# Optimization experiments

Measured on AMD Instinct MI355X. Metric: run time of the kernel, lower is better.

## Reference

```python
import jax, jax.numpy as jnp
import numpy as np

B, T, D = 8, 8192, 256
H = 16            # history_length
K = 3             # neighbor kernel_size
DECAY = 0.9
EPS = 1e-5


def _layernorm(x, g, b):
    m = jnp.mean(x, axis=-1, keepdims=True)
    v = jnp.var(x, axis=-1, keepdims=True)
    return (x - m) * jax.lax.rsqrt(v + EPS) * g + b


def _window_weighted_sum(x_pad, weights, seq_len):
    # sum_j w[j] * x_pad[:, j:j+T, :] -- fixed-weight local aggregation,
    # avoids materializing the [B,T,W,D] unfold tensor.
    out = weights[0] * x_pad[:, 0:seq_len, :]
    for j in range(1, weights.shape[0]):
        out = out + weights[j] * x_pad[:, j:j + seq_len, :]
    return out


def temporal_weights():
    w = DECAY ** np.arange(H, dtype=np.float32)
    return jnp.asarray(w / w.sum())


def setup_inputs() -> dict:
    key = jax.random.key(0)
    ks = jax.random.split(key, 16)
    s = 1.0 / np.sqrt(D)
    s2 = 1.0 / np.sqrt(2 * D)
    inp = {
        "x": jax.random.normal(ks[0], (B, T, D), jnp.float32),
        # LayerNorms
        "n1_g": jnp.ones((D,), jnp.float32), "n1_b": jnp.zeros((D,), jnp.float32),
        "n2_g": jnp.ones((D,), jnp.float32), "n2_b": jnp.zeros((D,), jnp.float32),
        "n3_g": jnp.ones((D,), jnp.float32), "n3_b": jnp.zeros((D,), jnp.float32),
        # temporal value/out proj (stored as [in,out])
        "t_Wv": jax.random.uniform(ks[1], (D, D), jnp.float32, -s, s),
        "t_bv": jax.random.uniform(ks[2], (D,), jnp.float32, -s, s),
        "t_Wo": jax.random.uniform(ks[3], (D, D), jnp.float32, -s, s),
        "t_bo": jax.random.uniform(ks[4], (D,), jnp.float32, -s, s),
        # neighbor value/out proj
        "a_Wv": jax.random.uniform(ks[5], (D, D), jnp.float32, -s, s),
        "a_bv": jax.random.uniform(ks[6], (D,), jnp.float32, -s, s),
        "a_Wo": jax.random.uniform(ks[7], (D, D), jnp.float32, -s, s),
        "a_bo": jax.random.uniform(ks[8], (D,), jnp.float32, -s, s),
        # FFN
        "f_W1": jax.random.uniform(ks[9], (D, 2 * D), jnp.float32, -s, s),
        "f_b1": jax.random.uniform(ks[10], (2 * D,), jnp.float32, -s, s),
        "f_W2": jax.random.uniform(ks[11], (2 * D, D), jnp.float32, -s2, s2),
        "f_b2": jax.random.uniform(ks[12], (D,), jnp.float32, -s2, s2),
    }
    return inp


def reference(x, n1_g, n1_b, n2_g, n2_b, n3_g, n3_b,
              t_Wv, t_bv, t_Wo, t_bo,
              a_Wv, a_bv, a_Wo, a_bo,
              f_W1, f_b1, f_W2, f_b2):
    # --- temporal memory: causal fixed exponential-decay window ---
    h = _layernorm(x, n1_g, n1_b)
    h_pad = jnp.pad(h, ((0, 0), (H - 1, 0), (0, 0)))  # zeros on the left
    tw = temporal_weights()  # tw[j] weights the j-th-oldest element (decay^j)
    agg = _window_weighted_sum(h_pad, tw, T)
    # weights sum to 1 => weighted-sum-of-linear == linear-of-weighted-sum
    attended = agg @ t_Wv + t_bv
    x = x + (attended @ t_Wo + t_bo)

    # --- neighbor attention: [t-1, t, t+1] uniform window, replicate pad ---
    h = _layernorm(x, n2_g, n2_b)
    h_pad = jnp.pad(h, ((0, 0), (1, 1), (0, 0)), mode="edge")
    nw = jnp.full((K,), 1.0 / K, jnp.float32)
    agg = _window_weighted_sum(h_pad, nw, T)
    attended = agg @ a_Wv + a_bv
    x = x + (attended @ a_Wo + a_bo)

    # --- FFN (dropout is identity at eval) ---
    h = _layernorm(x, n3_g, n3_b)
    h = jax.nn.gelu(h @ f_W1 + f_b1, approximate=False)
    x = x + (h @ f_W2 + f_b2)
    return x
```

## Files before the change

kernel.cpp:

```cpp
#include <hip/hip_runtime.h>
#include <cstdint>
#include <cstddef>

#define TT 8192
#define BB 8
#define DD 256
#define NTOK (BB * TT)

typedef unsigned short u16;
typedef unsigned int u32;

typedef __attribute__((ext_vector_type(8))) short bf16x8;
typedef __attribute__((ext_vector_type(4))) float f32x4;

__device__ __forceinline__ float bf2f(u16 u) {
    u32 v = ((u32)u) << 16;
    float f;
    __builtin_memcpy(&f, &v, 4);
    return f;
}

__device__ __forceinline__ u16 f2bf(float f) {
    u32 v;
    __builtin_memcpy(&v, &f, 4);
    u32 r = (v + 0x7FFFu + ((v >> 16) & 1u)) >> 16;
    return (u16)r;
}

__device__ __forceinline__ uint2 pack4(const float* v) {
    uint2 p;
    p.x = (u32)f2bf(v[0]) | ((u32)f2bf(v[1]) << 16);
    p.y = (u32)f2bf(v[2]) | ((u32)f2bf(v[3]) << 16);
    return p;
}

__device__ __forceinline__ void unpack4(uint2 p, float* v) {
    v[0] = bf2f((u16)(p.x & 0xFFFFu));
    v[1] = bf2f((u16)(p.x >> 16));
    v[2] = bf2f((u16)(p.y & 0xFFFFu));
    v[3] = bf2f((u16)(p.y >> 16));
}

__device__ __forceinline__ uint4 pack8(const float* v) {
    uint4 p;
    p.x = (u32)f2bf(v[0]) | ((u32)f2bf(v[1]) << 16);
    p.y = (u32)f2bf(v[2]) | ((u32)f2bf(v[3]) << 16);
    p.z = (u32)f2bf(v[4]) | ((u32)f2bf(v[5]) << 16);
    p.w = (u32)f2bf(v[6]) | ((u32)f2bf(v[7]) << 16);
    return p;
}

__device__ __forceinline__ void unpack8(uint4 p, float* v) {
    v[0] = bf2f((u16)(p.x & 0xFFFFu));
    v[1] = bf2f((u16)(p.x >> 16));
    v[2] = bf2f((u16)(p.y & 0xFFFFu));
    v[3] = bf2f((u16)(p.y >> 16));
    v[4] = bf2f((u16)(p.z & 0xFFFFu));
    v[5] = bf2f((u16)(p.z >> 16));
    v[6] = bf2f((u16)(p.w & 0xFFFFu));
    v[7] = bf2f((u16)(p.w >> 16));
}

__global__ __launch_bounds__(256) void k_diag(float* out, float code) {
    out[(size_t)blockIdx.x * 256 + threadIdx.x] = code;
}

__global__ __launch_bounds__(256) void k_transpose(
    const float* s0, const float* s1, const float* s2, const float* s3,
    const float* s4, const float* s5,
    u16* d0, u16* d1, u16* d2, u16* d3, u16* d4, u16* d5) {
    const int z = blockIdx.z;
    const float* src;
    u16* dst;
    int K, N, tr;
    switch (z) {
        case 0: src = s0; dst = d0; K = 256; N = 256; tr = 1; break;
        case 1: src = s1; dst = d1; K = 256; N = 256; tr = 1; break;
        case 2: src = s2; dst = d2; K = 256; N = 512; tr = 1; break;
        case 3: src = s3; dst = d3; K = 512; N = 256; tr = 1; break;
        case 4: src = s4; dst = d4; K = 256; N = 256; tr = 0; break;
        default: src = s5; dst = d5; K = 256; N = 256; tr = 0; break;
    }
    const int nb = blockIdx.x * 32, kb = blockIdx.y * 32;
    if (nb >= N || kb >= K) return;
    const int tx = threadIdx.x & 31, ty = threadIdx.x >> 5;
    if (!tr) {
        for (int i = ty; i < 32; i += 8)
            dst[(size_t)(kb + i) * N + nb + tx] =
                f2bf(src[(size_t)(kb + i) * N + nb + tx]);
        return;
    }
    __shared__ u16 tile[32][33];
    for (int i = ty; i < 32; i += 8)
        tile[i][tx] = f2bf(src[(size_t)(kb + i) * N + nb + tx]);
    __syncthreads();
    for (int i = ty; i < 32; i += 8)
        dst[(size_t)(nb + i) * K + kb + tx] = tile[tx][i];
}

__global__ __launch_bounds__(256) void k_bias_compose(
    const float* tbv, const float* tWo, const float* tbo,
    const float* abv, const float* aWo, const float* abo,
    float* bc1, float* bc2) {
    const float* bv = blockIdx.x ? abv : tbv;
    const float* Wo = blockIdx.x ? aWo : tWo;
    const float* bo = blockIdx.x ? abo : tbo;
    float* bc = blockIdx.x ? bc2 : bc1;
    const int n = threadIdx.x;
    float s = bo[n];
    for (int j = 0; j < 256; j++) s += bv[j] * Wo[j * 256 + n];
    bc[n] = s;
}

__global__ __launch_bounds__(256) void k_ln_temporal(
    const float* __restrict__ x, const float* __restrict__ gw,
    const float* __restrict__ bw, u16* __restrict__ out) {
    const int b = blockIdx.y;
    const int t0 = blockIdx.x * 64;
    const int tid = threadIdx.x;
    const int wv = tid >> 6, lane = tid & 63;
    const int d4 = lane * 4;
    __shared__ u16 hl[79 * 256];

    const float4 gv = *(const float4*)(gw + d4);
    const float4 bv = *(const float4*)(bw + d4);

    for (int i = wv; i < 79; i += 4) {
        const int t = t0 + i - 15;
        if (t < 0) {
            *(uint2*)(hl + i * 256 + d4) = make_uint2(0u, 0u);
            continue;
        }
        const float4 v = *(const float4*)(x + ((size_t)b * TT + t) * DD + d4);
        float s = v.x + v.y + v.z + v.w;
        float ss = v.x * v.x + v.y * v.y + v.z * v.z + v.w * v.w;
        for (int m = 1; m < 64; m <<= 1) {
            s += __shfl_xor(s, m);
            ss += __shfl_xor(ss, m);
        }
        const float mean = s * (1.0f / 256.0f);
        const float var = ss * (1.0f / 256.0f) - mean * mean;
        const float rs = rsqrtf(fmaxf(var, 0.f) + 1e-5f);
        float h[4] = {(v.x - mean) * rs * gv.x + bv.x,
                      (v.y - mean) * rs * gv.y + bv.y,
                      (v.z - mean) * rs * gv.z + bv.z,
                      (v.w - mean) * rs * gv.w + bv.w};
        *(uint2*)(hl + i * 256 + d4) = pack4(h);
    }
    __syncthreads();

    float tw[16];
    {
        float p = 1.f, s = 0.f;
        for (int j = 0; j < 16; j++) {
            tw[j] = p;
            s += p;
            p *= 0.9f;
        }
        const float inv = 1.f / s;
        for (int j = 0; j < 16; j++) tw[j] *= inv;
    }
    const int dc = (tid & 63) * 4;
    const int tg = (tid >> 6) * 16;
    for (int ot = tg; ot < tg + 16; ++ot) {
        float a[4] = {0.f, 0.f, 0.f, 0.f};
        for (int j = 0; j < 16; j++) {
            float h[4];
            unpack4(*(const uint2*)(hl + (ot + j) * 256 + dc), h);
            a[0] += tw[j] * h[0];
            a[1] += tw[j] * h[1];
            a[2] += tw[j] * h[2];
            a[3] += tw[j] * h[3];
        }
        *(uint2*)(out + ((size_t)b * TT + t0 + ot) * DD + dc) = pack4(a);
    }
}

__global__ __launch_bounds__(256) void k_gemm_prep(
    const u16* __restrict__ A, const u16* __restrict__ Wt,
    u16* out, int M, int K, int Nc, int ldw) {
    const int m0 = blockIdx.y * 128;
    const int n0 = blockIdx.x * 128;
    const int tid = threadIdx.x;
    const int wv = tid >> 6, lane = tid & 63;
    const int quad = lane >> 4, l16 = lane & 15;
    const int wm = (wv >> 1) * 64, wn = (wv & 1) * 64;

    __shared__ u16 lA[128 * 40];
    __shared__ u16 lB[128 * 40];

    f32x4 acc[4][4];
#pragma unroll
    for (int i = 0; i < 4; i++)
#pragma unroll
        for (int j = 0; j < 4; j++) acc[i][j] = (f32x4){0.f, 0.f, 0.f, 0.f};

    const int r = tid >> 2;
    const int c = tid & 3;

    for (int k0 = 0; k0 < K; k0 += 32) {
        __syncthreads();
        {
            const uint4 a0 = *(const uint4*)(A + (size_t)(m0 + r) * K + k0 + c * 8);
            const uint4 a1 = *(const uint4*)(A + (size_t)(m0 + r + 64) * K + k0 + c * 8);
            const uint4 b0 = *(const uint4*)(Wt + (size_t)(n0 + r) * ldw + k0 + c * 8);
            const uint4 b1 = *(const uint4*)(Wt + (size_t)(n0 + r + 64) * ldw + k0 + c * 8);
            *(uint4*)(lA + r * 40 + c * 8) = a0;
            *(uint4*)(lA + (r + 64) * 40 + c * 8) = a1;
            *(uint4*)(lB + r * 40 + c * 8) = b0;
            *(uint4*)(lB + (r + 64) * 40 + c * 8) = b1;
        }
        __syncthreads();
        bf16x8 af[4], bfr[4];
#pragma unroll
        for (int i = 0; i < 4; i++)
            af[i] = *(const bf16x8*)(lA + (wm + i * 16 + l16) * 40 + quad * 8);
#pragma unroll
        for (int j = 0; j < 4; j++)
            bfr[j] = *(const bf16x8*)(lB + (wn + j * 16 + l16) * 40 + quad * 8);
#pragma unroll
        for (int i = 0; i < 4; i++)
#pragma unroll
            for (int j = 0; j < 4; j++)
                acc[i][j] = __builtin_amdgcn_mfma_f32_16x16x32_bf16(
                    af[i], bfr[j], acc[i][j], 0, 0, 0);
    }

#pragma unroll
    for (int i = 0; i < 4; i++) {
        const int rowb = m0 + wm + i * 16 + quad * 4;
#pragma unroll
        for (int j = 0; j < 4; j++) {
            const int col = n0 + wn + j * 16 + l16;
#pragma unroll
            for (int rr = 0; rr < 4; rr++)
                out[(size_t)(rowb + rr) * Nc + col] = f2bf(acc[i][j][rr]);
        }
    }
}

template <int AMODE, int RES, int GELU, int SF32, int LNOUT>
__global__ __launch_bounds__(256) void k_mega(
    const u16* __restrict__ A, const u16* __restrict__ A2, int K,
    const u16* __restrict__ Wt, int ldw, const float* __restrict__ bias,
    const float* res, float* outf, u16* __restrict__ outh,
    const float* __restrict__ lng, const float* __restrict__ lnb,
    u16* __restrict__ hout) {
    const int m0 = blockIdx.x * 64;
    const int t = threadIdx.x;
    const int lane = t & 63, wv = t >> 6;
    const int quad = lane >> 4, l16 = lane & 15;
    const int wn = wv * 64;

    __shared__ u16 sA[66 * 40];
    __shared__ u16 sA2[AMODE ? 64 * 40 : 8];
    __shared__ float sBuf[5120];
    u16* sB = (u16*)sBuf;
    float* sE = sBuf;
    __shared__ float sMean[16], sRstd[16];
    __shared__ float sG[LNOUT ? 256 : 1], sBl[LNOUT ? 256 : 1];

    if (LNOUT) {
        sG[t] = lng[t];
        sBl[t] = lnb[t];
    }

    f32x4 acc[4][4];
#pragma unroll
    for (int i = 0; i < 4; i++)
#pragma unroll
        for (int j = 0; j < 4; j++) acc[i][j] = (f32x4){0.f, 0.f, 0.f, 0.f};

    int rowLo = 0, rowHi = 0;
    if (AMODE) {
        rowLo = (m0 % TT == 0) ? m0 : m0 - 1;
        rowHi = ((m0 + 64) % TT == 0) ? (m0 + 63) : (m0 + 64);
    }

    const int ar = t >> 2, ac8 = (t & 3) * 8;
    for (int k0 = 0; k0 < K; k0 += 32) {
        const u16* Asrc = (k0 >= 256) ? A2 : A;
        const int kk = k0 & 255;
        __syncthreads();
        if (AMODE == 0) {
            *(uint4*)(sA + ar * 40 + ac8) =
                *(const uint4*)(Asrc + (size_t)(m0 + ar) * 256 + kk + ac8);
        } else {
            *(uint4*)(sA + (ar + 1) * 40 + ac8) =
                *(const uint4*)(Asrc + (size_t)(m0 + ar) * 256 + kk + ac8);
            if (t < 8) {
                const int hr = (t >> 2) ? rowHi : rowLo;
                const int dr = (t >> 2) ? 65 : 0;
                *(uint4*)(sA + dr * 40 + (t & 3) * 8) =
                    *(const uint4*)(Asrc + (size_t)hr * 256 + kk + (t & 3) * 8);
            }
        }
#pragma unroll
        for (int q = 0; q < 4; q++) {
            const int ch = t + q * 256;
            *(uint4*)(sB + (ch >> 2) * 40 + (ch & 3) * 8) =
                *(const uint4*)(Wt + (size_t)(ch >> 2) * ldw + k0 + (ch & 3) * 8);
        }
        __syncthreads();
        if (AMODE) {
            float v0[8], v1[8], v2[8], o[8];
            unpack8(*(const uint4*)(sA + ar * 40 + ac8), v0);
            unpack8(*(const uint4*)(sA + (ar + 1) * 40 + ac8), v1);
            unpack8(*(const uint4*)(sA + (ar + 2) * 40 + ac8), v2);
#pragma unroll
            for (int e = 0; e < 8; e++)
                o[e] = (v0[e] + v1[e] + v2[e]) * (1.0f / 3.0f);
            *(uint4*)(sA2 + ar * 40 + ac8) = pack8(o);
            __syncthreads();
        }
        const u16* Af = AMODE ? sA2 : sA;
        bf16x8 af[4], bfr[4];
#pragma unroll
        for (int i = 0; i < 4; i++)
            af[i] = *(const bf16x8*)(Af + (i * 16 + l16) * 40 + quad * 8);
#pragma unroll
        for (int j = 0; j < 4; j++)
            bfr[j] = *(const bf16x8*)(sB + (wn + j * 16 + l16) * 40 + quad * 8);
#pragma unroll
        for (int i = 0; i < 4; i++)
#pragma unroll
            for (int j = 0; j < 4; j++)
                acc[i][j] = __builtin_amdgcn_mfma_f32_16x16x32_bf16(
                    af[i], bfr[j], acc[i][j], 0, 0, 0);
    }

    float bvl[4];
#pragma unroll
    for (int j = 0; j < 4; j++) bvl[j] = bias[wn + j * 16 + l16];

    const int row = t >> 4;
    const int colb = (t & 15) * 16;
    for (int cch = 0; cch < 4; cch++) {
        const int gr = m0 + cch * 16 + row;
        __syncthreads();
        if (RES) {
            const float* rp = res + (size_t)gr * 256 + colb;
            float* sp = sE + row * 268 + colb;
#pragma unroll
            for (int q = 0; q < 4; q++)
                *(float4*)(sp + q * 4) = *(const float4*)(rp + q * 4);
        }
        __syncthreads();
        {
#pragma unroll
            for (int j = 0; j < 4; j++) {
#pragma unroll
                for (int rr = 0; rr < 4; rr++) {
                    const int rl = quad * 4 + rr;
                    const int ad = rl * 268 + wn + j * 16 + l16;
                    float v = acc[cch][j][rr] + bvl[j];
                    if (RES) v += sE[ad];
                    if (GELU)
                        v = 0.5f * v * (1.0f + erff(v * 0.70710678118654752f));
                    sE[ad] = v;
                }
            }
        }
        __syncthreads();
        if (LNOUT) {
#pragma unroll
            for (int r4 = 0; r4 < 4; r4++) {
                const int rl = wv * 4 + r4;
                const float4 vv = *(const float4*)(sE + rl * 268 + lane * 4);
                float s = vv.x + vv.y + vv.z + vv.w;
                float ss = vv.x * vv.x + vv.y * vv.y + vv.z * vv.z + vv.w * vv.w;
                for (int m = 1; m < 64; m <<= 1) {
                    s += __shfl_xor(s, m);
                    ss += __shfl_xor(ss, m);
                }
                if (lane == 0) {
                    const float mean = s * (1.0f / 256.0f);
                    const float var = ss * (1.0f / 256.0f) - mean * mean;
                    sMean[rl] = mean;
                    sRstd[rl] = rsqrtf(fmaxf(var, 0.f) + 1e-5f);
                }
            }
            __syncthreads();
        }
        const float* sp = sE + row * 268 + colb;
        if (SF32) {
            float* op = outf + (size_t)gr * 256 + colb;
#pragma unroll
            for (int q = 0; q < 4; q++)
                *(float4*)(op + q * 4) = *(const float4*)(sp + q * 4);
        }
        if (GELU) {
            u16* op = outh + (size_t)gr * 256 + colb;
            *(uint4*)op = pack8(sp);
            *(uint4*)(op + 8) = pack8(sp + 8);
        }
        if (LNOUT) {
            const float m = sMean[row], rs = sRstd[row];
            float h[16];
#pragma unroll
            for (int e = 0; e < 16; e++)
                h[e] = (sp[e] - m) * rs * sG[colb + e] + sBl[colb + e];
            u16* hp = hout + (size_t)gr * 256 + colb;
            *(uint4*)hp = pack8(h);
            *(uint4*)(hp + 8) = pack8(h + 8);
        }
    }
}

__global__ __launch_bounds__(256) void k_ffn(
    const u16* __restrict__ A,
    const u16* __restrict__ W1T,
    const float* __restrict__ b1,
    const u16* __restrict__ W2T,
    const float* __restrict__ b2,
    const float* res,
    float* out) {
    const int m0 = blockIdx.x * 64;
    const int t = threadIdx.x;
    const int lane = t & 63, wv = t >> 6;
    const int quad = lane >> 4, l16 = lane & 15;

    __shared__ u16 sA[8 * 64 * 40];
    __shared__ u16 sT[64 * 72];
    float* sE = (float*)sA;

#pragma unroll
    for (int q = 0; q < 8; q++) {
        const int id = q * 256 + t;
        const int arow = id >> 5;
        const int c8 = (id & 31) * 8;
        const int ks = c8 >> 5;
        const int kc = c8 & 31;
        *(uint4*)(sA + (ks * 64 + arow) * 40 + kc) =
            *(const uint4*)(A + (size_t)(m0 + arow) * 256 + c8);
    }

    f32x4 acc2[4][4];
#pragma unroll
    for (int i = 0; i < 4; i++)
#pragma unroll
        for (int jj = 0; jj < 4; jj++) acc2[i][jj] = (f32x4){0.f, 0.f, 0.f, 0.f};

    __syncthreads();

    for (int j = 0; j < 8; j++) {
        const int n1 = j * 64 + wv * 16 + l16;
        bf16x8 bw[8];
#pragma unroll
        for (int ks = 0; ks < 8; ks++)
            bw[ks] = *(const bf16x8*)(W1T + (size_t)n1 * 256 + ks * 32 + quad * 8);
        f32x4 acc1[4];
#pragma unroll
        for (int i = 0; i < 4; i++) acc1[i] = (f32x4){0.f, 0.f, 0.f, 0.f};
#pragma unroll
        for (int ks = 0; ks < 8; ks++) {
#pragma unroll
            for (int i = 0; i < 4; i++) {
                const bf16x8 af = *(const bf16x8*)(
                    sA + (ks * 64 + i * 16 + l16) * 40 + quad * 8);
                acc1[i] = __builtin_amdgcn_mfma_f32_16x16x32_bf16(
                    af, bw[ks], acc1[i], 0, 0, 0);
            }
        }
        const float b1l = b1[n1];
#pragma unroll
        for (int i = 0; i < 4; i++)
#pragma unroll
            for (int rr = 0; rr < 4; rr++) {
                float v = acc1[i][rr] + b1l;
                v = 0.5f * v * (1.0f + erff(v * 0.70710678118654752f));
                sT[(i * 16 + quad * 4 + rr) * 72 + wv * 16 + l16] = f2bf(v);
            }
        __syncthreads();
#pragma unroll
        for (int kh = 0; kh < 2; kh++) {
            bf16x8 bw2[4];
#pragma unroll
            for (int jj = 0; jj < 4; jj++)
                bw2[jj] = *(const bf16x8*)(
                    W2T + (size_t)(wv * 64 + jj * 16 + l16) * 512 + j * 64 +
                    kh * 32 + quad * 8);
#pragma unroll
            for (int i = 0; i < 4; i++) {
                const bf16x8 af = *(const bf16x8*)(
                    sT + (i * 16 + l16) * 72 + kh * 32 + quad * 8);
#pragma unroll
                for (int jj = 0; jj < 4; jj++)
                    acc2[i][jj] = __builtin_amdgcn_mfma_f32_16x16x32_bf16(
                        af, bw2[jj], acc2[i][jj], 0, 0, 0);
            }
        }
        __syncthreads();
    }

    float bvl[4];
#pragma unroll
    for (int jj = 0; jj < 4; jj++) bvl[jj] = b2[wv * 64 + jj * 16 + l16];
    const int row = t >> 4;
    const int colb = (t & 15) * 16;
    for (int cch = 0; cch < 4; cch++) {
        const int gr = m0 + cch * 16 + row;
        __syncthreads();
        {
            const float* rp = res + (size_t)gr * 256 + colb;
            float* sp = sE + row * 268 + colb;
#pragma unroll
            for (int q = 0; q < 4; q++)
                *(float4*)(sp + q * 4) = *(const float4*)(rp + q * 4);
        }
        __syncthreads();
#pragma unroll
        for (int jj = 0; jj < 4; jj++)
#pragma unroll
            for (int rr = 0; rr < 4; rr++) {
                const int ad = (quad * 4 + rr) * 268 + wv * 64 + jj * 16 + l16;
                sE[ad] += acc2[cch][jj][rr] + bvl[jj];
            }
        __syncthreads();
        {
            float* op = out + (size_t)gr * 256 + colb;
            const float* sp = sE + row * 268 + colb;
#pragma unroll
            for (int q = 0; q < 4; q++)
                *(float4*)(op + q * 4) = *(const float4*)(sp + q * 4);
        }
    }
}

extern "C" void kernel_launch(void* const* d_in, const int* in_sizes, int n_in,
                              void* d_out, int out_size, void* d_ws,
                              size_t ws_size, hipStream_t stream) {
    const float* x = (const float*)d_in[0];
    const float* n1g = (const float*)d_in[1];
    const float* n1b = (const float*)d_in[2];
    const float* n2g = (const float*)d_in[3];
    const float* n2b = (const float*)d_in[4];
    const float* n3g = (const float*)d_in[5];
    const float* n3b = (const float*)d_in[6];
    const float* tWv = (const float*)d_in[7];
    const float* tbv = (const float*)d_in[8];
    const float* tWo = (const float*)d_in[9];
    const float* tbo = (const float*)d_in[10];
    const float* aWv = (const float*)d_in[11];
    const float* abv = (const float*)d_in[12];
    const float* aWo = (const float*)d_in[13];
    const float* abo = (const float*)d_in[14];
    const float* fW1 = (const float*)d_in[15];
    const float* fb1 = (const float*)d_in[16];
    const float* fW2 = (const float*)d_in[17];
    const float* fb2 = (const float*)d_in[18];
    float* outp = (float*)d_out;

    u16* wq = (u16*)d_ws;
    u16* tWoT = wq;
    u16* aWoT = wq + 65536;
    u16* fW1T = wq + 131072;
    u16* fW2T = wq + 262144;
    u16* WcT1 = wq + 393216;
    u16* WcT2 = wq + 458752;
    u16* tWvB = wq + 524288;
    u16* aWvB = wq + 589824;
    float* bc1 = (float*)(wq + 655360);
    float* bc2 = (float*)(wq + 655872);
    const size_t W_ELEMS = 656384;
    const size_t SLOT = (size_t)NTOK * 256;
    u16* slot1 = wq + W_ELEMS;
    u16* slot2 = slot1 + SLOT;
    u16* slot3 = slot2 + SLOT;

    const size_t need = (W_ELEMS + 3 * SLOT) * 2;
    if (ws_size < need) {
        k_diag<<<dim3(NTOK), 256, 0, stream>>>(outp,
                                               512.0f + (float)(ws_size >> 20));
        return;
    }

    k_transpose<<<dim3(16, 16, 6), 256, 0, stream>>>(
        tWo, aWo, fW1, fW2, tWv, aWv, tWoT, aWoT, fW1T, fW2T, tWvB, aWvB);
    k_gemm_prep<<<dim3(2, 2), 256, 0, stream>>>(tWoT, tWvB, WcT1, 256, 256,
                                                256, 256);
    k_gemm_prep<<<dim3(2, 2), 256, 0, stream>>>(aWoT, aWvB, WcT2, 256, 256,
                                                256, 256);
    k_bias_compose<<<dim3(2), 256, 0, stream>>>(tbv, tWo, tbo, abv, aWo, abo,
                                                bc1, bc2);

    const dim3 mg(NTOK / 64);

    k_ln_temporal<<<dim3(TT / 64, BB), 256, 0, stream>>>(x, n1g, n1b, slot1);

    k_mega<0, 1, 0, 1, 1><<<mg, 256, 0, stream>>>(
        slot1, slot1, 256, WcT1, 256, bc1, x, outp, nullptr, n2g, n2b, slot2);

    k_mega<1, 1, 0, 1, 1><<<mg, 256, 0, stream>>>(
        slot2, slot2, 256, WcT2, 256, bc2, outp, outp, nullptr, n3g, n3b,
        slot1);

    k_ffn<<<mg, 256, 0, stream>>>(slot1, fW1T, fb1, fW2T, fb2, outp, outp);
}
```

Baseline: 416.9 us.

## Stage full A tile once in LDS and read weights directly from global

The projection kernels now load the entire 64x256 activation tile into LDS in one pass, with the neighbor-average computed straight from global rows, and drop the per-K-step LDS staging of weights and its syncs. Weight fragments are read from global memory (L2/cached) directly into registers in each K step. The FFN kernel also hoists its W2 fragment loads ahead of the first GEMM so they overlap with compute. The aim is fewer barriers and less LDS traffic, at the cost of more LDS per block (about 40KB) and the neighbor mode reading three rows per element from global.

```diff
diff --git a/kernel.cpp b/kernel.cpp
--- a/kernel.cpp
+++ b/kernel.cpp
@@ -239,11 +239,13 @@
     }
 }
 
-template <int AMODE, int RES, int GELU, int SF32, int LNOUT>
-__global__ __launch_bounds__(256) void k_mega(
-    const u16* __restrict__ A, const u16* __restrict__ A2, int K,
-    const u16* __restrict__ Wt, int ldw, const float* __restrict__ bias,
-    const float* res, float* outf, u16* __restrict__ outh,
+template <int AMODE>
+__global__ __launch_bounds__(256) void k_mega2(
+    const u16* __restrict__ A,
+    const u16* __restrict__ Wt,
+    const float* __restrict__ bias,
+    const float* res,
+    float* outf,
     const float* __restrict__ lng, const float* __restrict__ lnb,
     u16* __restrict__ hout) {
     const int m0 = blockIdx.x * 64;
@@ -252,75 +254,58 @@
     const int quad = lane >> 4, l16 = lane & 15;
     const int wn = wv * 64;
 
-    __shared__ u16 sA[66 * 40];
-    __shared__ u16 sA2[AMODE ? 64 * 40 : 8];
-    __shared__ float sBuf[5120];
-    u16* sB = (u16*)sBuf;
-    float* sE = sBuf;
+    __shared__ u16 sA[8 * 64 * 40];
+    float* sE = (float*)sA;
     __shared__ float sMean[16], sRstd[16];
-    __shared__ float sG[LNOUT ? 256 : 1], sBl[LNOUT ? 256 : 1];
-
-    if (LNOUT) {
-        sG[t] = lng[t];
-        sBl[t] = lnb[t];
-    }
-
-    f32x4 acc[4][4];
-#pragma unroll
-    for (int i = 0; i < 4; i++)
-#pragma unroll
-        for (int j = 0; j < 4; j++) acc[i][j] = (f32x4){0.f, 0.f, 0.f, 0.f};
-
-    int rowLo = 0, rowHi = 0;
-    if (AMODE) {
-        rowLo = (m0 % TT == 0) ? m0 : m0 - 1;
-        rowHi = ((m0 + 64) % TT == 0) ? (m0 + 63) : (m0 + 64);
-    }
-
-    const int ar = t >> 2, ac8 = (t & 3) * 8;
-    for (int k0 = 0; k0 < K; k0 += 32) {
-        const u16* Asrc = (k0 >= 256) ? A2 : A;
-        const int kk = k0 & 255;
-        __syncthreads();
+    __shared__ float sG[256], sBl[256];
+
+    sG[t] = lng[t];
+    sBl[t] = lnb[t];
+
+#pragma unroll
+    for (int q = 0; q < 8; q++) {
+        const int id = q * 256 + t;
+        const int arow = id >> 5;
+        const int c8 = (id & 31) * 8;
+        const int ks = c8 >> 5;
+        const int kc = c8 & 31;
+        const int gr = m0 + arow;
         if (AMODE == 0) {
-            *(uint4*)(sA + ar * 40 + ac8) =
-                *(const uint4*)(Asrc + (size_t)(m0 + ar) * 256 + kk + ac8);
+            *(uint4*)(sA + (ks * 64 + arow) * 40 + kc) =
+                *(const uint4*)(A + (size_t)gr * 256 + c8);
         } else {
-            *(uint4*)(sA + (ar + 1) * 40 + ac8) =
-                *(const uint4*)(Asrc + (size_t)(m0 + ar) * 256 + kk + ac8);
-            if (t < 8) {
-                const int hr = (t >> 2) ? rowHi : rowLo;
-                const int dr = (t >> 2) ? 65 : 0;
-                *(uint4*)(sA + dr * 40 + (t & 3) * 8) =
-                    *(const uint4*)(Asrc + (size_t)hr * 256 + kk + (t & 3) * 8);
-            }
-        }
-#pragma unroll
-        for (int q = 0; q < 4; q++) {
-            const int ch = t + q * 256;
-            *(uint4*)(sB + (ch >> 2) * 40 + (ch & 3) * 8) =
-                *(const uint4*)(Wt + (size_t)(ch >> 2) * ldw + k0 + (ch & 3) * 8);
-        }
-        __syncthreads();
-        if (AMODE) {
+            const int rm = ((gr & (TT - 1)) == 0) ? gr : gr - 1;
+            const int rp = (((gr + 1) & (TT - 1)) == 0) ? gr : gr + 1;
             float v0[8], v1[8], v2[8], o[8];
-            unpack8(*(const uint4*)(sA + ar * 40 + ac8), v0);
-            unpack8(*(const uint4*)(sA + (ar + 1) * 40 + ac8), v1);
-            unpack8(*(const uint4*)(sA + (ar + 2) * 40 + ac8), v2);
+            unpack8(*(const uint4*)(A + (size_t)rm * 256 + c8), v0);
+            unpack8(*(const uint4*)(A + (size_t)gr * 256 + c8), v1);
+            unpack8(*(const uint4*)(A + (size_t)rp * 256 + c8), v2);
 #pragma unroll
             for (int e = 0; e < 8; e++)
                 o[e] = (v0[e] + v1[e] + v2[e]) * (1.0f / 3.0f);
-            *(uint4*)(sA2 + ar * 40 + ac8) = pack8(o);
-            __syncthreads();
-        }
-        const u16* Af = AMODE ? sA2 : sA;
-        bf16x8 af[4], bfr[4];
+            *(uint4*)(sA + (ks * 64 + arow) * 40 + kc) = pack8(o);
+        }
+    }
+
+    f32x4 acc[4][4];
+#pragma unroll
+    for (int i = 0; i < 4; i++)
+#pragma unroll
+        for (int j = 0; j < 4; j++) acc[i][j] = (f32x4){0.f, 0.f, 0.f, 0.f};
+
+    __syncthreads();
+
+#pragma unroll
+    for (int ks = 0; ks < 8; ks++) {
+        bf16x8 bfr[4], af[4];
+#pragma unroll
+        for (int j = 0; j < 4; j++)
+            bfr[j] = *(const bf16x8*)(Wt + (size_t)(wn + j * 16 + l16) * 256 +
+                                      ks * 32 + quad * 8);
 #pragma unroll
         for (int i = 0; i < 4; i++)
-            af[i] = *(const bf16x8*)(Af + (i * 16 + l16) * 40 + quad * 8);
-#pragma unroll
-        for (int j = 0; j < 4; j++)
-            bfr[j] = *(const bf16x8*)(sB + (wn + j * 16 + l16) * 40 + quad * 8);
+            af[i] = *(const bf16x8*)(sA + (ks * 64 + i * 16 + l16) * 40 +
+                                     quad * 8);
 #pragma unroll
         for (int i = 0; i < 4; i++)
 #pragma unroll
@@ -338,7 +323,7 @@
     for (int cch = 0; cch < 4; cch++) {
         const int gr = m0 + cch * 16 + row;
         __syncthreads();
-        if (RES) {
+        {
             const float* rp = res + (size_t)gr * 256 + colb;
             float* sp = sE + row * 268 + colb;
 #pragma unroll
@@ -346,55 +331,42 @@
                 *(float4*)(sp + q * 4) = *(const float4*)(rp + q * 4);
         }
         __syncthreads();
+#pragma unroll
+        for (int j = 0; j < 4; j++) {
+#pragma unroll
+            for (int rr = 0; rr < 4; rr++) {
+                const int rl = quad * 4 + rr;
+                const int ad = rl * 268 + wn + j * 16 + l16;
+                sE[ad] += acc[cch][j][rr] + bvl[j];
+            }
+        }
+        __syncthreads();
+#pragma unroll
+        for (int r4 = 0; r4 < 4; r4++) {
+            const int rl = wv * 4 + r4;
+            const float4 vv = *(const float4*)(sE + rl * 268 + lane * 4);
+            float s = vv.x + vv.y + vv.z + vv.w;
+            float ss = vv.x * vv.x + vv.y * vv.y + vv.z * vv.z + vv.w * vv.w;
+            for (int m = 1; m < 64; m <<= 1) {
+                s += __shfl_xor(s, m);
+                ss += __shfl_xor(ss, m);
+            }
+            if (lane == 0) {
+                const float mean = s * (1.0f / 256.0f);
+                const float var = ss * (1.0f / 256.0f) - mean * mean;
+                sMean[rl] = mean;
+                sRstd[rl] = rsqrtf(fmaxf(var, 0.f) + 1e-5f);
+            }
+        }
+        __syncthreads();
+        const float* sp = sE + row * 268 + colb;
         {
-#pragma unroll
-            for (int j = 0; j < 4; j++) {
-#pragma unroll
-                for (int rr = 0; rr < 4; rr++) {
-                    const int rl = quad * 4 + rr;
-                    const int ad = rl * 268 + wn + j * 16 + l16;
-                    float v = acc[cch][j][rr] + bvl[j];
-                    if (RES) v += sE[ad];
-                    if (GELU)
-                        v = 0.5f * v * (1.0f + erff(v * 0.70710678118654752f));
-                    sE[ad] = v;
-                }
-            }
-        }
-        __syncthreads();
-        if (LNOUT) {
-#pragma unroll
-            for (int r4 = 0; r4 < 4; r4++) {
-                const int rl = wv * 4 + r4;
-                const float4 vv = *(const float4*)(sE + rl * 268 + lane * 4);
-                float s = vv.x + vv.y + vv.z + vv.w;
-                float ss = vv.x * vv.x + vv.y * vv.y + vv.z * vv.z + vv.w * vv.w;
-                for (int m = 1; m < 64; m <<= 1) {
-                    s += __shfl_xor(s, m);
-                    ss += __shfl_xor(ss, m);
-                }
-                if (lane == 0) {
-                    const float mean = s * (1.0f / 256.0f);
-                    const float var = ss * (1.0f / 256.0f) - mean * mean;
-                    sMean[rl] = mean;
-                    sRstd[rl] = rsqrtf(fmaxf(var, 0.f) + 1e-5f);
-                }
-            }
-            __syncthreads();
-        }
-        const float* sp = sE + row * 268 + colb;
-        if (SF32) {
             float* op = outf + (size_t)gr * 256 + colb;
 #pragma unroll
             for (int q = 0; q < 4; q++)
                 *(float4*)(op + q * 4) = *(const float4*)(sp + q * 4);
         }
-        if (GELU) {
-            u16* op = outh + (size_t)gr * 256 + colb;
-            *(uint4*)op = pack8(sp);
-            *(uint4*)(op + 8) = pack8(sp + 8);
-        }
-        if (LNOUT) {
+        {
             const float m = sMean[row], rs = sRstd[row];
             float h[16];
 #pragma unroll
@@ -444,6 +416,14 @@
     __syncthreads();
 
     for (int j = 0; j < 8; j++) {
+        bf16x8 bw2[8];
+#pragma unroll
+        for (int kh = 0; kh < 2; kh++)
+#pragma unroll
+            for (int jj = 0; jj < 4; jj++)
+                bw2[kh * 4 + jj] = *(const bf16x8*)(
+                    W2T + (size_t)(wv * 64 + jj * 16 + l16) * 512 + j * 64 +
+                    kh * 32 + quad * 8);
         const int n1 = j * 64 + wv * 16 + l16;
         bf16x8 bw[8];
 #pragma unroll
@@ -474,12 +454,6 @@
         __syncthreads();
 #pragma unroll
         for (int kh = 0; kh < 2; kh++) {
-            bf16x8 bw2[4];
-#pragma unroll
-            for (int jj = 0; jj < 4; jj++)
-                bw2[jj] = *(const bf16x8*)(
-                    W2T + (size_t)(wv * 64 + jj * 16 + l16) * 512 + j * 64 +
-                    kh * 32 + quad * 8);
 #pragma unroll
             for (int i = 0; i < 4; i++) {
                 const bf16x8 af = *(const bf16x8*)(
@@ -487,7 +461,7 @@
 #pragma unroll
                 for (int jj = 0; jj < 4; jj++)
                     acc2[i][jj] = __builtin_amdgcn_mfma_f32_16x16x32_bf16(
-                        af, bw2[jj], acc2[i][jj], 0, 0, 0);
+                        af, bw2[kh * 4 + jj], acc2[i][jj], 0, 0, 0);
             }
         }
         __syncthreads();
@@ -588,12 +562,11 @@
 
     k_ln_temporal<<<dim3(TT / 64, BB), 256, 0, stream>>>(x, n1g, n1b, slot1);
 
-    k_mega<0, 1, 0, 1, 1><<<mg, 256, 0, stream>>>(
-        slot1, slot1, 256, WcT1, 256, bc1, x, outp, nullptr, n2g, n2b, slot2);
-
-    k_mega<1, 1, 0, 1, 1><<<mg, 256, 0, stream>>>(
-        slot2, slot2, 256, WcT2, 256, bc2, outp, outp, nullptr, n3g, n3b,
-        slot1);
+    k_mega2<0><<<mg, 256, 0, stream>>>(slot1, WcT1, bc1, x, outp, n2g, n2b,
+                                       slot2);
+
+    k_mega2<1><<<mg, 256, 0, stream>>>(slot2, WcT2, bc2, outp, outp, n3g, n3b,
+                                       slot1);
 
     k_ffn<<<mg, 256, 0, stream>>>(slot1, fW1T, fb1, fW2T, fb2, outp, outp);
 }
```

Measured after the change: 399.9 us. -4.1%, faster.
